# Kernel tuning notes

Measured on AMD Instinct MI355X. Metric: run time of the kernel, lower is better.

## Reference

```python
import jax, jax.numpy as jnp
import numpy as np

REF_MIC = 0
LOAD = 0.001 / np.sqrt(2.0)  # diagonal loading added to both real and imag parts


def _to_complex(x):
    # x: (N, 2, ...) real/imag stacked -> complex (N, ...)
    return x[:, 0] + 1j * x[:, 1]


def setup_inputs() -> dict:
    key = jax.random.key(0)
    k1, k2, k3 = jax.random.split(key, 3)
    N, C, T, F = 8, 16, 300, 257
    mixture = jax.random.normal(k1, (N, 2, C, T, F), dtype=jnp.float32)
    target = jax.random.normal(k2, (N, 2, C, T, F), dtype=jnp.float32)
    steering_vector = jax.random.normal(k3, (N, 2, C, F), dtype=jnp.float32)
    return {"mixture": mixture, "target": target, "steering_vector": steering_vector}


def reference(mixture, target, steering_vector):
    N, _, C, T, F = mixture.shape
    y = _to_complex(mixture)  # (N, C, T, F)
    x = _to_complex(target)   # (N, C, T, F)

    # Spatial covariance of mixture, mean over time frames (sum/T), fused einsum
    # phi[n,f] = (1/T) * sum_t y[n,:,t,f] y[n,:,t,f]^H  -> (N, F, C, C)
    phi = jnp.einsum('nctf,ndtf->nfcd', y, jnp.conj(y)) / T
    eye = jnp.eye(C, dtype=phi.dtype)
    # original adds load to BOTH real and imag diagonals (broadcast over RI dim)
    phi = phi + (LOAD + 1j * LOAD) * eye
    phi_inv = jnp.linalg.inv(phi)  # (N, F, C, C)

    # Cross covariance between mixture and reference-mic target
    A = jnp.transpose(y, (0, 3, 2, 1))            # (N, F, T, C)
    b = jnp.transpose(x[:, REF_MIC], (0, 2, 1))   # (N, F, T)
    mu_a = jnp.mean(A, axis=(0, 2), keepdims=True)  # mean over batch and time
    mu_b = jnp.mean(b, axis=(0, 2), keepdims=True)
    # mean over T of (A-mu_a)(b-mu_b)^H -> (N, F, C)
    phi_yx0 = jnp.mean((A - mu_a) * jnp.conj(b - mu_b)[..., None], axis=2)

    # MWF weights: w = phi_inv @ phi_yx0  -> (N, F, C)
    w = jnp.einsum('nfcd,nfd->nfc', phi_inv, phi_yx0)

    # Beamform: X_bf[n,t,f] = w[n,f]^H y[n,:,t,f]
    Xbf = jnp.einsum('nfc,nctf->ntf', jnp.conj(w), y)  # (N, T, F)

    # Back to real/imag stacked (N, 2, 1, T, F) matching torch output layout
    out = jnp.stack([Xbf.real, Xbf.imag], axis=1)[:, :, None]
    return out
```

## Files before the change

### kernel.cpp

```cpp
#include <hip/hip_runtime.h>

#define N_     8
#define C_     16
#define T_     300
#define F_     257
#define TF_    (T_*F_)
#define CTF_   (C_*TF_)
#define N2CTF_ (2*CTF_)

#define FT_    32
#define NFT_   9
#define TS_    5
#define SROW_  34
#define SSTG_  (SROW_*32)
#define SBUF_  (TS_*SSTG_)
#define NTILE_ 10
#define PHIC_  (NTILE_*16)

#define LOADC  7.0710678118654755e-04f

typedef float v2f __attribute__((ext_vector_type(2)));

__device__ __forceinline__ float2 cmul(float2 a, float2 b) {
  return make_float2(a.x*b.x - a.y*b.y, a.x*b.y + a.y*b.x);
}
__device__ __forceinline__ float2 cmulc(float2 a, float2 b) {
  return make_float2(a.x*b.x + a.y*b.y, a.y*b.x - a.x*b.y);
}
__device__ __forceinline__ float2 cdiv(float2 a, float2 b) {
  float inv = 1.0f / (b.x*b.x + b.y*b.y);
  return make_float2((a.x*b.x + a.y*b.y)*inv, (a.y*b.x - a.x*b.y)*inv);
}
__device__ __forceinline__ float2 cadd(float2 a, float2 b){ return make_float2(a.x+b.x, a.y+b.y); }
__device__ __forceinline__ float2 csub(float2 a, float2 b){ return make_float2(a.x-b.x, a.y-b.y); }

__device__ __forceinline__ void gload4(const float* g, float* l) {
  __builtin_amdgcn_global_load_lds(
      (const __attribute__((address_space(1))) unsigned int*)g,
      (__attribute__((address_space(3))) unsigned int*)l, 4, 0, 0);
}

template<int TCH>
__global__ __launch_bounds__(320) void k1_cov(const float* __restrict__ mix,
                                              const float* __restrict__ tgt,
                                              float2* __restrict__ phi_pf,
                                              float2* __restrict__ syx_pf,
                                              float2* __restrict__ sy_pf,
                                              float2* __restrict__ sx_pf) {
  __shared__ float ys[2 * SBUF_];
  v2f* phi_p = (v2f*)phi_pf;
  v2f* syx_p = (v2f*)syx_pf;
  v2f* sy_p  = (v2f*)sy_pf;
  v2f* sx_p  = (v2f*)sx_pf;
  const int tid = threadIdx.x;
  const int ft = blockIdx.x, tc = blockIdx.y, n = blockIdx.z;
  const int fbase = ft * FT_;
  const int t0 = tc * TCH;
  const int fl = tid & 31;
  const int g  = tid >> 5;
  int ti = 0, tj = g;
  while (tj > ti) { ++ti; tj -= ti; }
  const int c0 = ti * 4;
  const int d0 = tj * 4;
  const bool sThread = (tj == 0);

  const int w     = tid >> 6;
  const int plane = (tid >> 5) & 1;
  const int f_ld  = min(fbase + fl, F_ - 1);

  const float* mixN = mix + n * N2CTF_;
  const float* tgtN = tgt + n * N2CTF_;
  const float* ysrc = mixN + plane * CTF_ + (t0 + w) * F_ + f_ld;
  const float* xsrc = tgtN + plane * CTF_ + (t0 + w) * F_ + f_ld;

  v2f acc[4][4];
  #pragma unroll
  for (int i = 0; i < 4; ++i)
    #pragma unroll
    for (int j = 0; j < 4; ++j) acc[i][j] = (v2f){0.f, 0.f};
  v2f syx[4], sy[4], sx = (v2f){0.f, 0.f};
  #pragma unroll
  for (int i = 0; i < 4; ++i) { syx[i] = (v2f){0.f,0.f}; sy[i] = (v2f){0.f,0.f}; }

  constexpr int NS = TCH / TS_;
  static_assert(NS * TS_ == TCH, "TCH must be a multiple of TS_");

  {
    float* dst = &ys[w * SSTG_];
    #pragma unroll
    for (int c = 0; c < 16; ++c) gload4(ysrc + c * TF_, dst + 2 * c * 32);
    gload4(xsrc, dst + 32 * 32);
  }

  for (int s = 0; s < NS; ++s) {
    __syncthreads();
    if (s + 1 < NS) {
      float* dst = &ys[((s + 1) & 1) * SBUF_ + w * SSTG_];
      const float* yp = ysrc + (s + 1) * (TS_ * F_);
      #pragma unroll
      for (int c = 0; c < 16; ++c) gload4(yp + c * TF_, dst + 2 * c * 32);
      gload4(xsrc + (s + 1) * (TS_ * F_), dst + 32 * 32);
    }
    const float* bufc = &ys[(s & 1) * SBUF_];
    #pragma unroll
    for (int tl = 0; tl < TS_; ++tl) {
      const float* rt = bufc + tl * SSTG_;
      v2f a[4], bu[4], bv[4];
      #pragma unroll
      for (int i = 0; i < 4; ++i) {
        float re = rt[(2 * (c0 + i)) * 32 + fl];
        float im = rt[(2 * (c0 + i)) * 32 + 32 + fl];
        a[i] = (v2f){re, im};
      }
      #pragma unroll
      for (int j = 0; j < 4; ++j) {
        float re = rt[(2 * (d0 + j)) * 32 + fl];
        float im = rt[(2 * (d0 + j)) * 32 + 32 + fl];
        bu[j] = (v2f){re, -im};
        bv[j] = (v2f){im,  re};
      }
      #pragma unroll
      for (int i = 0; i < 4; ++i)
        #pragma unroll
        for (int j = 0; j < 4; ++j)
          acc[i][j] += a[i].x * bu[j] + a[i].y * bv[j];
      if (sThread) {
        float xre = rt[32 * 32 + fl];
        float xim = rt[33 * 32 + fl];
        v2f xu = (v2f){xre, -xim};
        v2f xw = (v2f){xim,  xre};
        #pragma unroll
        for (int i = 0; i < 4; ++i) {
          syx[i] += a[i].x * xu + a[i].y * xw;
          sy[i]  += a[i];
        }
        if (g == 0) sx += (v2f){xre, xim};
      }
    }
  }

  const int f = fbase + fl;
  if (f < F_) {
    const int tcn = tc * N_ + n;
    v2f* pb = phi_p + ((size_t)tcn * F_ + f) * PHIC_ + g * 16;
    #pragma unroll
    for (int i = 0; i < 4; ++i)
      #pragma unroll
      for (int j = 0; j < 4; ++j) pb[i * 4 + j] = acc[i][j];
    if (sThread) {
      v2f* s1 = syx_p + ((size_t)tcn * F_ + f) * C_ + c0;
      v2f* s2 = sy_p  + ((size_t)tcn * F_ + f) * C_ + c0;
      #pragma unroll
      for (int i = 0; i < 4; ++i) { s1[i] = syx[i]; s2[i] = sy[i]; }
      if (g == 0) sx_p[(size_t)tcn * F_ + f] = sx;
    }
  }
}

template<int TCP>
__global__ __launch_bounds__(256) void k2_fused(const float2* __restrict__ phi_p,
                                                const float2* __restrict__ syx_p,
                                                const float2* __restrict__ sy_p,
                                                const float2* __restrict__ sx_p,
                                                float* __restrict__ wre,
                                                float* __restrict__ wim) {
  __shared__ float2 ld_sy[TCP * N_ * C_];
  __shared__ float2 ld_syx[TCP * C_];
  __shared__ float2 ld_sx[TCP * N_];
  __shared__ float2 Msh[16 * 17];
  __shared__ float2 muB_s, sxO_s;
  const int f = blockIdx.x, n = blockIdx.y;
  const int tid = threadIdx.x;
  const int i = tid >> 4, j = tid & 15;

  const int ti = i >> 2, tj = j >> 2, ci = i & 3, cj = j & 3;
  int gL, cell; bool cj_flip;
  if (ti >= tj) { gL = ti * (ti + 1) / 2 + tj; cell = ci * 4 + cj; cj_flip = false; }
  else          { gL = tj * (tj + 1) / 2 + ti; cell = cj * 4 + ci; cj_flip = true; }
  const int off = gL * 16 + cell;

  float2 s = make_float2(0.f, 0.f);
  for (int tc = 0; tc < TCP; ++tc) {
    float2 v = phi_p[((size_t)(tc * N_ + n) * F_ + f) * PHIC_ + off];
    s.x += v.x; s.y += v.y;
  }
  if (cj_flip) s.y = -s.y;
  if (i == j) { s.x += (float)T_ * LOADC; s.y += (float)T_ * LOADC; }

  for (int idx = tid; idx < TCP * N_ * C_; idx += 256) {
    int tcn = idx >> 4, c = idx & 15;
    ld_sy[idx] = sy_p[((size_t)tcn * F_ + f) * C_ + c];
  }
  for (int idx = tid; idx < TCP * C_; idx += 256) {
    int tc = idx >> 4, c = idx & 15;
    ld_syx[idx] = syx_p[((size_t)(tc * N_ + n) * F_ + f) * C_ + c];
  }
  for (int idx = tid; idx < TCP * N_; idx += 256) {
    ld_sx[idx] = sx_p[(size_t)idx * F_ + f];
  }
  __syncthreads();

  float2 muA_r = make_float2(0.f,0.f), ownY = make_float2(0.f,0.f), ownYX = make_float2(0.f,0.f);
  if (tid < 16) {
    float2 allY = make_float2(0.f,0.f);
    for (int tcn = 0; tcn < TCP * N_; ++tcn) allY = cadd(allY, ld_sy[tcn * C_ + tid]);
    for (int tc = 0; tc < TCP; ++tc) {
      ownY  = cadd(ownY,  ld_sy[(tc * N_ + n) * C_ + tid]);
      ownYX = cadd(ownYX, ld_syx[tc * C_ + tid]);
    }
    const float invNT = 1.0f / ((float)N_ * (float)T_);
    muA_r = make_float2(allY.x * invNT, allY.y * invNT);
  }
  if (tid == 16) {
    float2 own = make_float2(0.f,0.f), all = make_float2(0.f,0.f);
    for (int tc = 0; tc < TCP; ++tc)
      for (int nn = 0; nn < N_; ++nn) {
        float2 v = ld_sx[tc * N_ + nn];
        all = cadd(all, v);
        if (nn == n) own = cadd(own, v);
      }
    const float invNT = 1.0f / ((float)N_ * (float)T_);
    muB_s = make_float2(all.x * invNT, all.y * invNT);
    sxO_s = own;
  }
  __syncthreads();

  Msh[i * 17 + j] = s;
  if (tid < 16) {
    float2 r = ownYX;
    r = csub(r, cmulc(muA_r, sxO_s));
    r = csub(r, cmulc(ownY, muB_s));
    float2 t3 = cmulc(muA_r, muB_s);
    r.x += (float)T_ * t3.x; r.y += (float)T_ * t3.y;
    Msh[tid * 17 + 16] = r;
  }
  __syncthreads();

  for (int k = 0; k < 16; ++k) {
    float2 fac = cdiv(Msh[i * 17 + k], Msh[k * 17 + k]);
    __syncthreads();
    if (i != k) {
      Msh[i * 17 + j] = csub(Msh[i * 17 + j], cmul(fac, Msh[k * 17 + j]));
      if (j == 15) Msh[i * 17 + 16] = csub(Msh[i * 17 + 16], cmul(fac, Msh[k * 17 + 16]));
    }
    __syncthreads();
  }
  if (j == 0) {
    float2 wv = cdiv(Msh[i * 17 + 16], Msh[i * 17 + i]);
    wre[(n * C_ + i) * F_ + f] = wv.x;
    wim[(n * C_ + i) * F_ + f] = wv.y;
  }
}

__global__ __launch_bounds__(320) void k3_bf(const float* __restrict__ mix,
                                             const float* __restrict__ wre,
                                             const float* __restrict__ wim,
                                             float* __restrict__ out) {
  const int t0 = blockIdx.x * 2, n = blockIdx.y;
  const int f = threadIdx.x;
  if (f >= F_) return;
  const float* mixN = mix + n * N2CTF_;
  const float* wR = wre + n * C_ * F_;
  const float* wI = wim + n * C_ * F_;
  float* outN = out + n * 2 * TF_;
  float wr[16], wi[16];
  #pragma unroll
  for (int c = 0; c < 16; ++c) { wr[c] = wR[c * F_ + f]; wi[c] = wI[c * F_ + f]; }
  const float* yb = mixN + t0 * F_ + f;
  float xr0 = 0.f, xi0 = 0.f, xr1 = 0.f, xi1 = 0.f;
  #pragma unroll
  for (int c = 0; c < 16; ++c) {
    float yr0 = yb[c * TF_],      yi0 = yb[CTF_ + c * TF_];
    float yr1 = yb[c * TF_ + F_], yi1 = yb[CTF_ + c * TF_ + F_];
    xr0 += wr[c] * yr0 + wi[c] * yi0;
    xi0 += wr[c] * yi0 - wi[c] * yr0;
    xr1 += wr[c] * yr1 + wi[c] * yi1;
    xi1 += wr[c] * yi1 - wi[c] * yr1;
  }
  outN[t0 * F_ + f] = xr0;
  outN[TF_ + t0 * F_ + f] = xi0;
  outN[(t0 + 1) * F_ + f] = xr1;
  outN[TF_ + (t0 + 1) * F_ + f] = xi1;
}

template<int TCP>
static void launch_all(const float* mix, const float* tgt, float* ws, float* out,
                       hipStream_t stream) {
  constexpr int TCH = T_ / TCP;
  static_assert(TCH * TCP == T_ && TCH % TS_ == 0, "chunking");
  float2* phi_p = (float2*)ws;
  float2* syx_p = phi_p + (size_t)TCP * N_ * F_ * PHIC_;
  float2* sy_p  = syx_p + (size_t)TCP * N_ * F_ * C_;
  float2* sx_p  = sy_p  + (size_t)TCP * N_ * F_ * C_;
  float*  wre   = (float*)(sx_p + (size_t)TCP * N_ * F_);
  float*  wim   = wre + N_ * C_ * F_;
  k1_cov<TCH><<<dim3(NFT_, TCP, N_), dim3(320), 0, stream>>>(mix, tgt, phi_p, syx_p, sy_p, sx_p);
  k2_fused<TCP><<<dim3(F_, N_), dim3(256), 0, stream>>>(phi_p, syx_p, sy_p, sx_p, wre, wim);
  k3_bf<<<dim3(T_ / 2, N_), dim3(320), 0, stream>>>(mix, wre, wim, out);
}

static size_t ws_need_bytes(int tcp) {
  size_t fl2 = (size_t)tcp * N_ * F_ * (PHIC_ + 2 * C_ + 1);
  return fl2 * 8 + 2ull * N_ * C_ * F_ * 4;
}

extern "C" void kernel_launch(void* const* d_in, const int* in_sizes, int n_in,
                              void* d_out, int out_size, void* d_ws, size_t ws_size,
                              hipStream_t stream) {
  const float* mix = (const float*)d_in[0];
  const float* tgt = (const float*)d_in[1];
  float* out = (float*)d_out;
  float* ws  = (float*)d_ws;
  if (ws_size >= ws_need_bytes(12))      launch_all<12>(mix, tgt, ws, out, stream);
  else if (ws_size >= ws_need_bytes(10)) launch_all<10>(mix, tgt, ws, out, stream);
  else if (ws_size >= ws_need_bytes(2))  launch_all<2>(mix, tgt, ws, out, stream);
  else                                   launch_all<1>(mix, tgt, ws, out, stream);
}
```

Baseline: 227.6 us.

## Restructure beamforming kernel with double-buffered async LDS staging over time chunks

The beamforming kernel now tiles over 32 frequency bins and 30-frame time chunks. Each wave stages one frame's real or imaginary plane for all 16 channels into LDS using async gload4 copies, double-buffered so the next stage loads while the current one computes. Weights are loaded once per block and reused across the 30 frames, and each thread computes either the real or the imaginary output. The host dispatcher also stops using the 12-way time split for the covariance kernel and picks 10 as the largest, which changes that kernel's grid.

```diff
diff --git a/kernel.cpp b/kernel.cpp
--- a/kernel.cpp
+++ b/kernel.cpp
@@ -16,6 +16,10 @@
 #define SBUF_  (TS_*SSTG_)
 #define NTILE_ 10
 #define PHIC_  (NTILE_*16)
+
+#define TS3_   5
+#define SSTG3_ (32*32)
+#define SBUF3_ (TS3_*SSTG3_)
 
 #define LOADC  7.0710678118654755e-04f
 
@@ -252,35 +256,65 @@
   }
 }
 
+template<int TCH3>
 __global__ __launch_bounds__(320) void k3_bf(const float* __restrict__ mix,
                                              const float* __restrict__ wre,
                                              const float* __restrict__ wim,
                                              float* __restrict__ out) {
-  const int t0 = blockIdx.x * 2, n = blockIdx.y;
-  const int f = threadIdx.x;
-  if (f >= F_) return;
-  const float* mixN = mix + n * N2CTF_;
-  const float* wR = wre + n * C_ * F_;
-  const float* wI = wim + n * C_ * F_;
+  __shared__ float ys[2 * SBUF3_];
+  const int tid = threadIdx.x;
+  const int ft = blockIdx.x, tc = blockIdx.y, n = blockIdx.z;
+  const int fbase = ft * FT_;
+  const int t0 = tc * TCH3;
+  const int fl = tid & 31;
+  const int plane = (tid >> 5) & 1;
+  const int w = tid >> 6;
+  const int f_ld = min(fbase + fl, F_ - 1);
+
+  const float* ysrc = mix + n * N2CTF_ + plane * CTF_ + (t0 + w) * F_ + f_ld;
+
+  float wr[16], wi[16];
+  {
+    const float* wR = wre + n * C_ * F_ + f_ld;
+    const float* wI = wim + n * C_ * F_ + f_ld;
+    #pragma unroll
+    for (int c = 0; c < 16; ++c) { wr[c] = wR[c * F_]; wi[c] = wI[c * F_]; }
+  }
+
   float* outN = out + n * 2 * TF_;
-  float wr[16], wi[16];
-  #pragma unroll
-  for (int c = 0; c < 16; ++c) { wr[c] = wR[c * F_ + f]; wi[c] = wI[c * F_ + f]; }
-  const float* yb = mixN + t0 * F_ + f;
-  float xr0 = 0.f, xi0 = 0.f, xr1 = 0.f, xi1 = 0.f;
-  #pragma unroll
-  for (int c = 0; c < 16; ++c) {
-    float yr0 = yb[c * TF_],      yi0 = yb[CTF_ + c * TF_];
-    float yr1 = yb[c * TF_ + F_], yi1 = yb[CTF_ + c * TF_ + F_];
-    xr0 += wr[c] * yr0 + wi[c] * yi0;
-    xi0 += wr[c] * yi0 - wi[c] * yr0;
-    xr1 += wr[c] * yr1 + wi[c] * yi1;
-    xi1 += wr[c] * yi1 - wi[c] * yr1;
-  }
-  outN[t0 * F_ + f] = xr0;
-  outN[TF_ + t0 * F_ + f] = xi0;
-  outN[(t0 + 1) * F_ + f] = xr1;
-  outN[TF_ + (t0 + 1) * F_ + f] = xi1;
+  const int f = fbase + fl;
+
+  constexpr int NS = TCH3 / TS3_;
+  static_assert(NS * TS3_ == TCH3, "TCH3 must be a multiple of TS3_");
+
+  {
+    float* dst = &ys[w * SSTG3_];
+    #pragma unroll
+    for (int c = 0; c < 16; ++c) gload4(ysrc + c * TF_, dst + 2 * c * 32);
+  }
+
+  for (int s = 0; s < NS; ++s) {
+    __syncthreads();
+    if (s + 1 < NS) {
+      float* dst = &ys[((s + 1) & 1) * SBUF3_ + w * SSTG3_];
+      const float* yp = ysrc + (s + 1) * (TS3_ * F_);
+      #pragma unroll
+      for (int c = 0; c < 16; ++c) gload4(yp + c * TF_, dst + 2 * c * 32);
+    }
+    const float* rt = &ys[(s & 1) * SBUF3_ + w * SSTG3_];
+    float s1 = 0.f, s2 = 0.f;
+    #pragma unroll
+    for (int c = 0; c < 16; ++c) {
+      float yr = rt[2 * c * 32 + fl];
+      float yi = rt[2 * c * 32 + 32 + fl];
+      s1 += wr[c] * yr + wi[c] * yi;
+      s2 += wr[c] * yi - wi[c] * yr;
+    }
+    if (f < F_) {
+      const int t = t0 + s * TS3_ + w;
+      outN[t * F_ + f + plane * TF_] = plane ? s2 : s1;
+    }
+  }
 }
 
 template<int TCP>
@@ -296,7 +330,8 @@
   float*  wim   = wre + N_ * C_ * F_;
   k1_cov<TCH><<<dim3(NFT_, TCP, N_), dim3(320), 0, stream>>>(mix, tgt, phi_p, syx_p, sy_p, sx_p);
   k2_fused<TCP><<<dim3(F_, N_), dim3(256), 0, stream>>>(phi_p, syx_p, sy_p, sx_p, wre, wim);
-  k3_bf<<<dim3(T_ / 2, N_), dim3(320), 0, stream>>>(mix, wre, wim, out);
+  constexpr int TCH3 = 30;
+  k3_bf<TCH3><<<dim3(NFT_, T_ / TCH3, N_), dim3(320), 0, stream>>>(mix, wre, wim, out);
 }
 
 static size_t ws_need_bytes(int tcp) {
@@ -311,8 +346,7 @@
   const float* tgt = (const float*)d_in[1];
   float* out = (float*)d_out;
   float* ws  = (float*)d_ws;
-  if (ws_size >= ws_need_bytes(12))      launch_all<12>(mix, tgt, ws, out, stream);
-  else if (ws_size >= ws_need_bytes(10)) launch_all<10>(mix, tgt, ws, out, stream);
-  else if (ws_size >= ws_need_bytes(2))  launch_all<2>(mix, tgt, ws, out, stream);
-  else                                   launch_all<1>(mix, tgt, ws, out, stream);
-}
+  if (ws_size >= ws_need_bytes(10))     launch_all<10>(mix, tgt, ws, out, stream);
+  else if (ws_size >= ws_need_bytes(2)) launch_all<2>(mix, tgt, ws, out, stream);
+  else                                  launch_all<1>(mix, tgt, ws, out, stream);
+}
```

After: 230.1 us. No clear change (+1.1%).

## Solve all batch items per frequency in one block of the solve kernel

Applied to the files above, without the earlier changes.

The solve kernel now launches one block per frequency instead of one per (frequency, batch). Each block holds all eight 16x16 augmented systems in shared memory and runs Gauss-Jordan elimination over them together. The per-frequency sums of sy and sx are therefore loaded and reduced once rather than eight times, and the barrier cost is shared across the batch. In exchange the grid drops from about 2056 blocks to 257 and shared memory per block grows, so fewer waves are in flight to hide latency. The temporal chunk count is capped at 10, likely to keep shared-memory use within limits.

```diff
diff --git a/kernel.cpp b/kernel.cpp
--- a/kernel.cpp
+++ b/kernel.cpp
@@ -158,20 +158,31 @@
 }
 
 template<int TCP>
-__global__ __launch_bounds__(256) void k2_fused(const float2* __restrict__ phi_p,
+__global__ __launch_bounds__(256) void k2_solve(const float2* __restrict__ phi_p,
                                                 const float2* __restrict__ syx_p,
                                                 const float2* __restrict__ sy_p,
                                                 const float2* __restrict__ sx_p,
                                                 float* __restrict__ wre,
                                                 float* __restrict__ wim) {
   __shared__ float2 ld_sy[TCP * N_ * C_];
-  __shared__ float2 ld_syx[TCP * C_];
+  __shared__ float2 ld_syx[TCP * N_ * C_];
   __shared__ float2 ld_sx[TCP * N_];
-  __shared__ float2 Msh[16 * 17];
-  __shared__ float2 muB_s, sxO_s;
-  const int f = blockIdx.x, n = blockIdx.y;
+  __shared__ float2 Msh[N_ * 272];
+  __shared__ float2 muA_s[C_];
+  __shared__ float2 sxO_s[N_];
+  __shared__ float2 muB_s;
+  const int f = blockIdx.x;
   const int tid = threadIdx.x;
   const int i = tid >> 4, j = tid & 15;
+
+  for (int idx = tid; idx < TCP * N_ * C_; idx += 256) {
+    const size_t gsrc = ((size_t)(idx >> 4) * F_ + f) * C_ + (idx & 15);
+    ld_sy[idx]  = sy_p[gsrc];
+    ld_syx[idx] = syx_p[gsrc];
+  }
+  for (int idx = tid; idx < TCP * N_; idx += 256) {
+    ld_sx[idx] = sx_p[(size_t)idx * F_ + f];
+  }
 
   const int ti = i >> 2, tj = j >> 2, ci = i & 3, cj = j & 3;
   int gL, cell; bool cj_flip;
@@ -179,76 +190,87 @@
   else          { gL = tj * (tj + 1) / 2 + ti; cell = cj * 4 + ci; cj_flip = true; }
   const int off = gL * 16 + cell;
 
-  float2 s = make_float2(0.f, 0.f);
-  for (int tc = 0; tc < TCP; ++tc) {
-    float2 v = phi_p[((size_t)(tc * N_ + n) * F_ + f) * PHIC_ + off];
-    s.x += v.x; s.y += v.y;
-  }
-  if (cj_flip) s.y = -s.y;
-  if (i == j) { s.x += (float)T_ * LOADC; s.y += (float)T_ * LOADC; }
-
-  for (int idx = tid; idx < TCP * N_ * C_; idx += 256) {
-    int tcn = idx >> 4, c = idx & 15;
-    ld_sy[idx] = sy_p[((size_t)tcn * F_ + f) * C_ + c];
-  }
-  for (int idx = tid; idx < TCP * C_; idx += 256) {
-    int tc = idx >> 4, c = idx & 15;
-    ld_syx[idx] = syx_p[((size_t)(tc * N_ + n) * F_ + f) * C_ + c];
-  }
-  for (int idx = tid; idx < TCP * N_; idx += 256) {
-    ld_sx[idx] = sx_p[(size_t)idx * F_ + f];
+  #pragma unroll
+  for (int n = 0; n < N_; ++n) {
+    float2 s = make_float2(0.f, 0.f);
+    for (int tc = 0; tc < TCP; ++tc) {
+      float2 v = phi_p[((size_t)(tc * N_ + n) * F_ + f) * PHIC_ + off];
+      s.x += v.x; s.y += v.y;
+    }
+    if (cj_flip) s.y = -s.y;
+    if (i == j) { s.x += (float)T_ * LOADC; s.y += (float)T_ * LOADC; }
+    Msh[n * 272 + i * 17 + j] = s;
   }
   __syncthreads();
 
-  float2 muA_r = make_float2(0.f,0.f), ownY = make_float2(0.f,0.f), ownYX = make_float2(0.f,0.f);
-  if (tid < 16) {
+  float2 ownY = make_float2(0.f,0.f), ownYX = make_float2(0.f,0.f);
+  const int sn = tid >> 4, sc = tid & 15;
+  if (tid < 128) {
+    const int n = sn;
+    for (int tc = 0; tc < TCP; ++tc) {
+      ownY  = cadd(ownY,  ld_sy[(tc * N_ + n) * C_ + sc]);
+      ownYX = cadd(ownYX, ld_syx[(tc * N_ + n) * C_ + sc]);
+    }
+  } else if (tid < 144) {
+    const int c = tid - 128;
     float2 allY = make_float2(0.f,0.f);
-    for (int tcn = 0; tcn < TCP * N_; ++tcn) allY = cadd(allY, ld_sy[tcn * C_ + tid]);
-    for (int tc = 0; tc < TCP; ++tc) {
-      ownY  = cadd(ownY,  ld_sy[(tc * N_ + n) * C_ + tid]);
-      ownYX = cadd(ownYX, ld_syx[tc * C_ + tid]);
-    }
+    for (int tcn = 0; tcn < TCP * N_; ++tcn) allY = cadd(allY, ld_sy[tcn * C_ + c]);
     const float invNT = 1.0f / ((float)N_ * (float)T_);
-    muA_r = make_float2(allY.x * invNT, allY.y * invNT);
-  }
-  if (tid == 16) {
-    float2 own = make_float2(0.f,0.f), all = make_float2(0.f,0.f);
+    muA_s[c] = make_float2(allY.x * invNT, allY.y * invNT);
+  } else if (tid == 144) {
+    float2 all = make_float2(0.f,0.f);
     for (int tc = 0; tc < TCP; ++tc)
-      for (int nn = 0; nn < N_; ++nn) {
-        float2 v = ld_sx[tc * N_ + nn];
-        all = cadd(all, v);
-        if (nn == n) own = cadd(own, v);
-      }
+      for (int nn = 0; nn < N_; ++nn) all = cadd(all, ld_sx[tc * N_ + nn]);
     const float invNT = 1.0f / ((float)N_ * (float)T_);
     muB_s = make_float2(all.x * invNT, all.y * invNT);
-    sxO_s = own;
+  } else if (tid < 153) {
+    const int n = tid - 145;
+    float2 own = make_float2(0.f,0.f);
+    for (int tc = 0; tc < TCP; ++tc) own = cadd(own, ld_sx[tc * N_ + n]);
+    sxO_s[n] = own;
   }
   __syncthreads();
 
-  Msh[i * 17 + j] = s;
-  if (tid < 16) {
+  if (tid < 128) {
+    const int n = sn;
     float2 r = ownYX;
-    r = csub(r, cmulc(muA_r, sxO_s));
+    r = csub(r, cmulc(muA_s[sc], sxO_s[n]));
     r = csub(r, cmulc(ownY, muB_s));
-    float2 t3 = cmulc(muA_r, muB_s);
+    float2 t3 = cmulc(muA_s[sc], muB_s);
     r.x += (float)T_ * t3.x; r.y += (float)T_ * t3.y;
-    Msh[tid * 17 + 16] = r;
+    Msh[n * 272 + sc * 17 + 16] = r;
   }
   __syncthreads();
 
   for (int k = 0; k < 16; ++k) {
-    float2 fac = cdiv(Msh[i * 17 + k], Msh[k * 17 + k]);
+    float2 fac[N_];
+    #pragma unroll
+    for (int n = 0; n < N_; ++n)
+      fac[n] = cdiv(Msh[n * 272 + i * 17 + k], Msh[n * 272 + k * 17 + k]);
     __syncthreads();
     if (i != k) {
-      Msh[i * 17 + j] = csub(Msh[i * 17 + j], cmul(fac, Msh[k * 17 + j]));
-      if (j == 15) Msh[i * 17 + 16] = csub(Msh[i * 17 + 16], cmul(fac, Msh[k * 17 + 16]));
+      #pragma unroll
+      for (int n = 0; n < N_; ++n) {
+        Msh[n * 272 + i * 17 + j] =
+            csub(Msh[n * 272 + i * 17 + j], cmul(fac[n], Msh[n * 272 + k * 17 + j]));
+      }
+      if (j == 15) {
+        #pragma unroll
+        for (int n = 0; n < N_; ++n) {
+          Msh[n * 272 + i * 17 + 16] =
+              csub(Msh[n * 272 + i * 17 + 16], cmul(fac[n], Msh[n * 272 + k * 17 + 16]));
+        }
+      }
     }
     __syncthreads();
   }
   if (j == 0) {
-    float2 wv = cdiv(Msh[i * 17 + 16], Msh[i * 17 + i]);
-    wre[(n * C_ + i) * F_ + f] = wv.x;
-    wim[(n * C_ + i) * F_ + f] = wv.y;
+    #pragma unroll
+    for (int n = 0; n < N_; ++n) {
+      float2 wv = cdiv(Msh[n * 272 + i * 17 + 16], Msh[n * 272 + i * 17 + i]);
+      wre[(n * C_ + i) * F_ + f] = wv.x;
+      wim[(n * C_ + i) * F_ + f] = wv.y;
+    }
   }
 }
 
@@ -295,7 +317,7 @@
   float*  wre   = (float*)(sx_p + (size_t)TCP * N_ * F_);
   float*  wim   = wre + N_ * C_ * F_;
   k1_cov<TCH><<<dim3(NFT_, TCP, N_), dim3(320), 0, stream>>>(mix, tgt, phi_p, syx_p, sy_p, sx_p);
-  k2_fused<TCP><<<dim3(F_, N_), dim3(256), 0, stream>>>(phi_p, syx_p, sy_p, sx_p, wre, wim);
+  k2_solve<TCP><<<dim3(F_), dim3(256), 0, stream>>>(phi_p, syx_p, sy_p, sx_p, wre, wim);
   k3_bf<<<dim3(T_ / 2, N_), dim3(320), 0, stream>>>(mix, wre, wim, out);
 }
 
@@ -311,8 +333,7 @@
   const float* tgt = (const float*)d_in[1];
   float* out = (float*)d_out;
   float* ws  = (float*)d_ws;
-  if (ws_size >= ws_need_bytes(12))      launch_all<12>(mix, tgt, ws, out, stream);
-  else if (ws_size >= ws_need_bytes(10)) launch_all<10>(mix, tgt, ws, out, stream);
-  else if (ws_size >= ws_need_bytes(2))  launch_all<2>(mix, tgt, ws, out, stream);
-  else                                   launch_all<1>(mix, tgt, ws, out, stream);
-}
+  if (ws_size >= ws_need_bytes(10))     launch_all<10>(mix, tgt, ws, out, stream);
+  else if (ws_size >= ws_need_bytes(2)) launch_all<2>(mix, tgt, ws, out, stream);
+  else                                  launch_all<1>(mix, tgt, ws, out, stream);
+}
```

After: 231.7 us. Within noise of the previous version (+1.8%).

## Reduce time-chunk partial covariances with atomics instead of per-chunk buffers

Applied to the files above, without the earlier changes.

k1 now accumulates its per-time-chunk covariance, cross-covariance and sum partials directly into a single per-(n,f) buffer using unsafe float atomic adds, after a memset clears the workspace. k2 then reads one reduced value instead of looping over TCP chunk partials and staging them in shared memory. This cuts the partial-buffer write and read traffic by the chunk factor and shrinks the workspace. In exchange it adds a memset launch and atomic contention, makes the summation order nondeterministic, and fixes TCP at 10 where the old code picked 12 when the workspace allowed.

```diff
diff --git a/kernel.cpp b/kernel.cpp
--- a/kernel.cpp
+++ b/kernel.cpp
@@ -40,18 +40,19 @@
       (__attribute__((address_space(3))) unsigned int*)l, 4, 0, 0);
 }
 
+__device__ __forceinline__ void aadd(float* p, float v) { unsafeAtomicAdd(p, v); }
+__device__ __forceinline__ void aadd2(float2* p, v2f v) {
+  unsafeAtomicAdd(&p->x, v.x); unsafeAtomicAdd(&p->y, v.y);
+}
+
 template<int TCH>
 __global__ __launch_bounds__(320) void k1_cov(const float* __restrict__ mix,
                                               const float* __restrict__ tgt,
-                                              float2* __restrict__ phi_pf,
-                                              float2* __restrict__ syx_pf,
-                                              float2* __restrict__ sy_pf,
-                                              float2* __restrict__ sx_pf) {
+                                              float2* __restrict__ phi_p,
+                                              float2* __restrict__ syx_p,
+                                              float2* __restrict__ sy_p,
+                                              float2* __restrict__ sx_p) {
   __shared__ float ys[2 * SBUF_];
-  v2f* phi_p = (v2f*)phi_pf;
-  v2f* syx_p = (v2f*)syx_pf;
-  v2f* sy_p  = (v2f*)sy_pf;
-  v2f* sx_p  = (v2f*)sx_pf;
   const int tid = threadIdx.x;
   const int ft = blockIdx.x, tc = blockIdx.y, n = blockIdx.z;
   const int fbase = ft * FT_;
@@ -141,32 +142,27 @@
 
   const int f = fbase + fl;
   if (f < F_) {
-    const int tcn = tc * N_ + n;
-    v2f* pb = phi_p + ((size_t)tcn * F_ + f) * PHIC_ + g * 16;
+    float2* pb = phi_p + ((size_t)(n * F_ + f)) * PHIC_ + g * 16;
     #pragma unroll
     for (int i = 0; i < 4; ++i)
       #pragma unroll
-      for (int j = 0; j < 4; ++j) pb[i * 4 + j] = acc[i][j];
+      for (int j = 0; j < 4; ++j) aadd2(pb + i * 4 + j, acc[i][j]);
     if (sThread) {
-      v2f* s1 = syx_p + ((size_t)tcn * F_ + f) * C_ + c0;
-      v2f* s2 = sy_p  + ((size_t)tcn * F_ + f) * C_ + c0;
-      #pragma unroll
-      for (int i = 0; i < 4; ++i) { s1[i] = syx[i]; s2[i] = sy[i]; }
-      if (g == 0) sx_p[(size_t)tcn * F_ + f] = sx;
-    }
-  }
-}
-
-template<int TCP>
+      float2* s1 = syx_p + ((size_t)(n * F_ + f)) * C_ + c0;
+      float2* s2 = sy_p  + ((size_t)(n * F_ + f)) * C_ + c0;
+      #pragma unroll
+      for (int i = 0; i < 4; ++i) { aadd2(s1 + i, syx[i]); aadd2(s2 + i, sy[i]); }
+      if (g == 0) aadd2(sx_p + (size_t)n * F_ + f, sx);
+    }
+  }
+}
+
 __global__ __launch_bounds__(256) void k2_fused(const float2* __restrict__ phi_p,
                                                 const float2* __restrict__ syx_p,
                                                 const float2* __restrict__ sy_p,
                                                 const float2* __restrict__ sx_p,
                                                 float* __restrict__ wre,
                                                 float* __restrict__ wim) {
-  __shared__ float2 ld_sy[TCP * N_ * C_];
-  __shared__ float2 ld_syx[TCP * C_];
-  __shared__ float2 ld_sx[TCP * N_];
   __shared__ float2 Msh[16 * 17];
   __shared__ float2 muB_s, sxO_s;
   const int f = blockIdx.x, n = blockIdx.y;
@@ -179,53 +175,30 @@
   else          { gL = tj * (tj + 1) / 2 + ti; cell = cj * 4 + ci; cj_flip = true; }
   const int off = gL * 16 + cell;
 
-  float2 s = make_float2(0.f, 0.f);
-  for (int tc = 0; tc < TCP; ++tc) {
-    float2 v = phi_p[((size_t)(tc * N_ + n) * F_ + f) * PHIC_ + off];
-    s.x += v.x; s.y += v.y;
-  }
+  float2 s = phi_p[((size_t)(n * F_ + f)) * PHIC_ + off];
   if (cj_flip) s.y = -s.y;
   if (i == j) { s.x += (float)T_ * LOADC; s.y += (float)T_ * LOADC; }
-
-  for (int idx = tid; idx < TCP * N_ * C_; idx += 256) {
-    int tcn = idx >> 4, c = idx & 15;
-    ld_sy[idx] = sy_p[((size_t)tcn * F_ + f) * C_ + c];
-  }
-  for (int idx = tid; idx < TCP * C_; idx += 256) {
-    int tc = idx >> 4, c = idx & 15;
-    ld_syx[idx] = syx_p[((size_t)(tc * N_ + n) * F_ + f) * C_ + c];
-  }
-  for (int idx = tid; idx < TCP * N_; idx += 256) {
-    ld_sx[idx] = sx_p[(size_t)idx * F_ + f];
-  }
-  __syncthreads();
+  Msh[i * 17 + j] = s;
 
   float2 muA_r = make_float2(0.f,0.f), ownY = make_float2(0.f,0.f), ownYX = make_float2(0.f,0.f);
   if (tid < 16) {
     float2 allY = make_float2(0.f,0.f);
-    for (int tcn = 0; tcn < TCP * N_; ++tcn) allY = cadd(allY, ld_sy[tcn * C_ + tid]);
-    for (int tc = 0; tc < TCP; ++tc) {
-      ownY  = cadd(ownY,  ld_sy[(tc * N_ + n) * C_ + tid]);
-      ownYX = cadd(ownYX, ld_syx[tc * C_ + tid]);
-    }
+    for (int nn = 0; nn < N_; ++nn)
+      allY = cadd(allY, sy_p[((size_t)(nn * F_ + f)) * C_ + tid]);
+    ownY  = sy_p[((size_t)(n * F_ + f)) * C_ + tid];
+    ownYX = syx_p[((size_t)(n * F_ + f)) * C_ + tid];
     const float invNT = 1.0f / ((float)N_ * (float)T_);
     muA_r = make_float2(allY.x * invNT, allY.y * invNT);
   }
   if (tid == 16) {
-    float2 own = make_float2(0.f,0.f), all = make_float2(0.f,0.f);
-    for (int tc = 0; tc < TCP; ++tc)
-      for (int nn = 0; nn < N_; ++nn) {
-        float2 v = ld_sx[tc * N_ + nn];
-        all = cadd(all, v);
-        if (nn == n) own = cadd(own, v);
-      }
+    float2 all = make_float2(0.f,0.f);
+    for (int nn = 0; nn < N_; ++nn) all = cadd(all, sx_p[(size_t)nn * F_ + f]);
     const float invNT = 1.0f / ((float)N_ * (float)T_);
     muB_s = make_float2(all.x * invNT, all.y * invNT);
-    sxO_s = own;
+    sxO_s = sx_p[(size_t)n * F_ + f];
   }
   __syncthreads();
 
-  Msh[i * 17 + j] = s;
   if (tid < 16) {
     float2 r = ownYX;
     r = csub(r, cmulc(muA_r, sxO_s));
@@ -283,25 +256,21 @@
   outN[TF_ + (t0 + 1) * F_ + f] = xi1;
 }
 
-template<int TCP>
+#define SUMF2_ ((size_t)N_ * F_ * (PHIC_ + 2 * C_ + 1))
+
 static void launch_all(const float* mix, const float* tgt, float* ws, float* out,
                        hipStream_t stream) {
-  constexpr int TCH = T_ / TCP;
-  static_assert(TCH * TCP == T_ && TCH % TS_ == 0, "chunking");
+  constexpr int TCP = 10, TCH = T_ / TCP;
   float2* phi_p = (float2*)ws;
-  float2* syx_p = phi_p + (size_t)TCP * N_ * F_ * PHIC_;
-  float2* sy_p  = syx_p + (size_t)TCP * N_ * F_ * C_;
-  float2* sx_p  = sy_p  + (size_t)TCP * N_ * F_ * C_;
-  float*  wre   = (float*)(sx_p + (size_t)TCP * N_ * F_);
+  float2* syx_p = phi_p + (size_t)N_ * F_ * PHIC_;
+  float2* sy_p  = syx_p + (size_t)N_ * F_ * C_;
+  float2* sx_p  = sy_p  + (size_t)N_ * F_ * C_;
+  float*  wre   = (float*)(sx_p + (size_t)N_ * F_);
   float*  wim   = wre + N_ * C_ * F_;
+  hipMemsetAsync(ws, 0, SUMF2_ * sizeof(float2), stream);
   k1_cov<TCH><<<dim3(NFT_, TCP, N_), dim3(320), 0, stream>>>(mix, tgt, phi_p, syx_p, sy_p, sx_p);
-  k2_fused<TCP><<<dim3(F_, N_), dim3(256), 0, stream>>>(phi_p, syx_p, sy_p, sx_p, wre, wim);
+  k2_fused<<<dim3(F_, N_), dim3(256), 0, stream>>>(phi_p, syx_p, sy_p, sx_p, wre, wim);
   k3_bf<<<dim3(T_ / 2, N_), dim3(320), 0, stream>>>(mix, wre, wim, out);
-}
-
-static size_t ws_need_bytes(int tcp) {
-  size_t fl2 = (size_t)tcp * N_ * F_ * (PHIC_ + 2 * C_ + 1);
-  return fl2 * 8 + 2ull * N_ * C_ * F_ * 4;
 }
 
 extern "C" void kernel_launch(void* const* d_in, const int* in_sizes, int n_in,
@@ -309,10 +278,5 @@
                               hipStream_t stream) {
   const float* mix = (const float*)d_in[0];
   const float* tgt = (const float*)d_in[1];
-  float* out = (float*)d_out;
-  float* ws  = (float*)d_ws;
-  if (ws_size >= ws_need_bytes(12))      launch_all<12>(mix, tgt, ws, out, stream);
-  else if (ws_size >= ws_need_bytes(10)) launch_all<10>(mix, tgt, ws, out, stream);
-  else if (ws_size >= ws_need_bytes(2))  launch_all<2>(mix, tgt, ws, out, stream);
-  else                                   launch_all<1>(mix, tgt, ws, out, stream);
-}
+  launch_all(mix, tgt, (float*)d_ws, (float*)d_out, stream);
+}
```

After: 600.8 us. 164% more time.
